# Optimization experiments

Measured on AMD Instinct MI355X. Metric: run time of the kernel, lower is better.

## Reference

```python
import jax, jax.numpy as jnp
import numpy as np

B, K, H, T, V = 32, 5, 512, 256, 5000
MAX_LEN = 64
SOS, EOS, PAD = 1, 2, 0
NEG = -1e9
ALPHA, MIN_LEN = 1.2, 5.0
SCALE = 1.0 / float(np.sqrt(H))


def setup_inputs() -> dict:
    key = jax.random.key(0)
    ks = jax.random.split(key, 5)
    s = 0.02
    return {
        "input_var": jnp.full((B, 1), SOS, dtype=jnp.int32),
        "encoder_outputs": jax.random.normal(ks[0], (B, T, H), dtype=jnp.float32),
        "emb_table": jax.random.normal(ks[1], (V, H), dtype=jnp.float32) * s,
        "w_ih": jax.random.normal(ks[2], (H, 3 * H), dtype=jnp.float32) * s,
        "w_hh": jax.random.normal(ks[3], (H, 3 * H), dtype=jnp.float32) * s,
        "w_out": jax.random.normal(ks[4], (2 * H, V), dtype=jnp.float32) * s,
        "k": K,
    }


def _gru_cell(x, h, w_ih, w_hh):
    iz, ir, inn = jnp.split(x @ w_ih, 3, axis=-1)
    hz, hr, hn = jnp.split(h @ w_hh, 3, axis=-1)
    z = jax.nn.sigmoid(iz + hz)
    r = jax.nn.sigmoid(ir + hr)
    n = jnp.tanh(inn + r * hn)
    return (1.0 - z) * n + z * h


def _forward_step(tok, h, enc, emb_table, w_ih, w_hh, w_out):
    # tok: [N] int, h: [N,H], enc: [N,T,H] -> (log-probs [N,V], new hidden [N,H])
    x = emb_table[tok]
    h = _gru_cell(x, h, w_ih, w_hh)
    att = jax.nn.softmax(jnp.einsum("nh,nth->nt", h, enc) * SCALE, axis=-1)
    ctx = jnp.einsum("nt,nth->nh", att, enc)
    logits = jnp.concatenate([h, ctx], axis=-1) @ w_out
    return jax.nn.log_softmax(logits, axis=-1), h


def reference(input_var, encoder_outputs, emb_table, w_ih, w_hh, w_out, k):
    bsz = encoder_outputs.shape[0]
    f32 = encoder_outputs.dtype

    # --- first step on un-inflated batch (hidden starts at zeros) ---
    h0 = jnp.zeros((bsz, H), dtype=f32)
    lp0, h1 = _forward_step(input_var[:, 0], h0, encoder_outputs,
                            emb_table, w_ih, w_hh, w_out)
    cum, beams = jax.lax.top_k(lp0, k)            # [B,k], [B,k]

    # inflate encoder states / hidden to beam-major layout [B*k, ...]
    enc_k = jnp.repeat(encoder_outputs, k, axis=0)   # [B*k,T,H]
    h = jnp.repeat(h1, k, axis=0)                    # [B*k,H]

    tokens = jnp.zeros((bsz, k, MAX_LEN), dtype=jnp.int32)
    tokens = tokens.at[:, :, 0].set(beams)
    finished = beams == EOS
    lengths = jnp.ones((bsz, k), dtype=jnp.int32)
    # finished beams may only extend with PAD at zero added log-prob
    pad_lp = jnp.where(jnp.arange(V) == PAD, 0.0, NEG).astype(f32)

    def body(carry, di):
        tokens, last, cum, h, finished, lengths = carry
        lp, h_new = _forward_step(last.reshape(-1), h, enc_k,
                                  emb_table, w_ih, w_hh, w_out)
        lp = lp.reshape(bsz, k, V)
        lp = jnp.where(finished[:, :, None], pad_lp[None, None, :], lp)
        # joint top-k over k*V candidates == per-beam topk(k) then topk over k^2
        cand = (cum[:, :, None] + lp).reshape(bsz, k * V)
        scores, idx = jax.lax.top_k(cand, k)      # [B,k]
        beam_ids = idx // V
        tok_ids = idx % V
        tokens = jnp.take_along_axis(tokens, beam_ids[:, :, None], axis=1)
        tokens = tokens.at[:, :, di].set(tok_ids)
        prev_fin = jnp.take_along_axis(finished, beam_ids, axis=1)
        lengths = jnp.take_along_axis(lengths, beam_ids, axis=1) + jnp.where(prev_fin, 0, 1)
        finished = prev_fin | (tok_ids == EOS)
        h = jnp.take_along_axis(h_new.reshape(bsz, k, H),
                                beam_ids[:, :, None], axis=1).reshape(bsz * k, H)
        return (tokens, tok_ids, scores, h, finished, lengths), None

    carry = (tokens, beams.astype(jnp.int32), cum, h, finished, lengths)
    (tokens, _, cum, _, finished, lengths), _ = jax.lax.scan(
        body, carry, jnp.arange(1, MAX_LEN))

    # length penalty on finished hypotheses, then pick best beam per batch
    penalty = ((MIN_LEN + lengths.astype(f32)) / (MIN_LEN + 1.0)) ** ALPHA
    sel = jnp.where(finished, cum / penalty, cum)
    best = jnp.argmax(sel, axis=1)
    hypothesis = jnp.take_along_axis(tokens, best[:, None, None], axis=1)[:, 0, :]
    return hypothesis, cum
```

## Files before the change

kernel.cpp:

```cpp
#include <hip/hip_runtime.h>
#include <math.h>

#define BB     32
#define KBM    5
#define NR     160
#define HD     512
#define TT     256
#define VV     5000
#define MAXLEN 64
#define EOSID  2
#define NEGV   (-1e9f)
#define NEGBIG (-3.0e38f)
#define SCALEF 0.04419417382415922f
#define NBLK   256
#define NTHR   512

typedef float v4f __attribute__((ext_vector_type(4)));

__device__ __forceinline__ float ld_sysf(const float* p) {
  return __hip_atomic_load(p, __ATOMIC_RELAXED, __HIP_MEMORY_SCOPE_SYSTEM);
}
__device__ __forceinline__ void st_sysf(float* p, float v) {
  __hip_atomic_store(p, v, __ATOMIC_RELAXED, __HIP_MEMORY_SCOPE_SYSTEM);
}
__device__ __forceinline__ int ld_sysi(const int* p) {
  return __hip_atomic_load(p, __ATOMIC_RELAXED, __HIP_MEMORY_SCOPE_SYSTEM);
}
__device__ __forceinline__ void st_sysi(int* p, int v) {
  __hip_atomic_store(p, v, __ATOMIC_RELAXED, __HIP_MEMORY_SCOPE_SYSTEM);
}
__device__ __forceinline__ v4f ld4_sys(const float* p) {
  v4f v;
  asm volatile("global_load_dwordx4 %0, %1, off sc0 sc1\n\ts_waitcnt vmcnt(0)"
               : "=v"(v) : "v"(p) : "memory");
  return v;
}
__device__ __forceinline__ void st4_sys(float* p, v4f v) {
  asm volatile("global_store_dwordx4 %0, %1, off sc0 sc1" :: "v"(p), "v"(v) : "memory");
}

__device__ __forceinline__ bool viBetter(float av, int ai, float bv, int bi) {
  return (av > bv) || (av == bv && ai < bi);
}

__device__ __forceinline__ void top5_insert(float tv[5], int ti[5], float x, int v) {
  if (!viBetter(x, v, tv[4], ti[4])) return;
  tv[4] = x; ti[4] = v;
#pragma unroll
  for (int q = 4; q > 0; q--) {
    if (viBetter(tv[q], ti[q], tv[q - 1], ti[q - 1])) {
      float tf = tv[q - 1]; int tx2 = ti[q - 1];
      tv[q - 1] = tv[q]; ti[q - 1] = ti[q];
      tv[q] = tf; ti[q] = tx2;
    } else break;
  }
}

template<int LEVELS>
__device__ __forceinline__ void bfly_argmax(float& v, int& i) {
#pragma unroll
  for (int d = 1; d < (1 << LEVELS); d <<= 1) {
    float ov = __shfl_xor(v, d);
    int oi = __shfl_xor(i, d);
    if (viBetter(ov, oi, v, i)) { v = ov; i = oi; }
  }
}

__global__ void k_zero(unsigned int* bar) {
  if (threadIdx.x < 320)
    __hip_atomic_store(&bar[threadIdx.x], 0u, __ATOMIC_RELAXED, __HIP_MEMORY_SCOPE_SYSTEM);
}

__launch_bounds__(NTHR, 1)
__global__ void k_persist(const int* __restrict__ input_var, const float* __restrict__ enc,
                          const float* __restrict__ emb, const float* __restrict__ w_ih,
                          const float* __restrict__ w_hh, const float* __restrict__ w_out,
                          float* __restrict__ out,
                          float* h, float* A_cat,
                          float* sumM, float* sumS, float* sumV, int* sumI,
                          int* last_tok, unsigned int* bar) {
  const int bid = blockIdx.x;
  const int tid = threadIdx.x;
  unsigned int ep = 0;

  __shared__ float sh_xs[32][40];
  __shared__ float sh_hs[32][40];
  __shared__ float sh_ws[6][32][32];
  __shared__ int   sh_toks[32];
  __shared__ float sh_h5[KBM][HD];
  __shared__ float sh_part[2][KBM][TT];
  __shared__ float sh_sc5[KBM][TT];
  __shared__ float sh_tmp5[KBM][TT];
  __shared__ float sh_as[32][72];
  __shared__ float sh_bs[64][136];
  __shared__ float sh_candV[KBM * KBM]; __shared__ int sh_candI[KBM * KBM];
  __shared__ int   sh_tokens[KBM][MAXLEN];
  __shared__ float sh_cum[KBM];
  __shared__ int   sh_fin[KBM]; __shared__ int sh_len[KBM];
  __shared__ float sh_oc[KBM];  __shared__ int sh_ofin[KBM]; __shared__ int sh_olen[KBM];
  __shared__ int   sh_ttmp[KBM * MAXLEN];
  __shared__ int   sh_selI[KBM]; __shared__ float sh_selV[KBM];

  auto gbar = [&]() {
    asm volatile("s_waitcnt vmcnt(0)" ::: "memory");
    __syncthreads();
    ep += 1;
    if (tid == 0) {
      __hip_atomic_fetch_add(&bar[(bid & 7) * 32], 1u, __ATOMIC_RELAXED,
                             __HIP_MEMORY_SCOPE_SYSTEM);
      if (bid == 0) {
        for (int c = 0; c < 8; c++) {
          while (__hip_atomic_load(&bar[c * 32], __ATOMIC_RELAXED,
                                   __HIP_MEMORY_SCOPE_SYSTEM) < ep * 32u) {
            __builtin_amdgcn_s_sleep(1);
          }
        }
        __hip_atomic_store(&bar[288], ep, __ATOMIC_RELAXED, __HIP_MEMORY_SCOPE_SYSTEM);
      } else {
        while (__hip_atomic_load(&bar[288], __ATOMIC_RELAXED,
                                 __HIP_MEMORY_SCOPE_SYSTEM) < ep) {
          __builtin_amdgcn_s_sleep(2);
        }
      }
    }
    __syncthreads();
  };

  if (bid < BB) {
    if (tid < KBM) { sh_cum[tid] = 0.f; sh_fin[tid] = 0; sh_len[tid] = 0; }
    for (int t = tid; t < KBM * MAXLEN; t += NTHR) sh_tokens[t >> 6][t & 63] = 0;
  }
  {
    int gidx = bid * NTHR + tid;
    v4f z4; z4[0] = z4[1] = z4[2] = z4[3] = 0.f;
    for (int i = gidx; i < NR * HD / 4; i += NBLK * NTHR) st4_sys(&h[i * 4], z4);
    for (int t = gidx; t < NR; t += NBLK * NTHR) st_sysi(&last_tok[t], input_var[t / KBM]);
  }
  gbar();

  for (int di = 0; di < MAXLEN; di++) {
    if (bid < 80) {
      const int bx = bid & 15, by = bid >> 4;
      const int i0 = bx * 32, n0 = by * 32;
      const int tx = tid & 31, ty = tid >> 5;
      if (tid < 32) sh_toks[tid] = ld_sysi(&last_tok[n0 + tid]);
      float acc[6][2];
#pragma unroll
      for (int g = 0; g < 6; g++) { acc[g][0] = 0.f; acc[g][1] = 0.f; }

      for (int k0 = 0; k0 < HD; k0 += 32) {
        __syncthreads();
#pragma unroll
        for (int p = 0; p < 4; p++) {
          int idx = tid + p * NTHR;
          if (idx < 256) {
            int r = idx >> 3, c4 = (idx & 7) * 4;
            *(v4f*)&sh_xs[r][c4] =
                *(const v4f*)&emb[(size_t)sh_toks[r] * HD + k0 + c4];
          } else if (idx < 512) {
            int r = (idx - 256) >> 3, c4 = ((idx - 256) & 7) * 4;
            *(v4f*)&sh_hs[r][c4] = ld4_sys(&h[(size_t)(n0 + r) * HD + k0 + c4]);
          } else {
            int widx = idx - 512;
            int g = widx >> 8, rem = widx & 255;
            int kk = rem >> 3, c4 = (rem & 7) * 4;
            const float* W = (g < 3) ? w_ih : w_hh;
            int gc = (g < 3) ? g : g - 3;
            *(v4f*)&sh_ws[g][kk][c4] =
                *(const v4f*)&W[(size_t)(k0 + kk) * 1536 + gc * HD + i0 + c4];
          }
        }
        __syncthreads();
#pragma unroll 8
        for (int k = 0; k < 32; k++) {
          float w0 = sh_ws[0][k][tx], w1 = sh_ws[1][k][tx], w2 = sh_ws[2][k][tx];
          float w3 = sh_ws[3][k][tx], w4 = sh_ws[4][k][tx], w5 = sh_ws[5][k][tx];
#pragma unroll
          for (int rr = 0; rr < 2; rr++) {
            float xv = sh_xs[ty * 2 + rr][k];
            float hv = sh_hs[ty * 2 + rr][k];
            acc[0][rr] += xv * w0; acc[1][rr] += xv * w1; acc[2][rr] += xv * w2;
            acc[3][rr] += hv * w3; acc[4][rr] += hv * w4; acc[5][rr] += hv * w5;
          }
        }
      }
#pragma unroll
      for (int rr = 0; rr < 2; rr++) {
        int n = n0 + ty * 2 + rr, i = i0 + tx;
        float hv = ld_sysf(&h[(size_t)n * HD + i]);
        float z = 1.f / (1.f + expf(-(acc[0][rr] + acc[3][rr])));
        float r = 1.f / (1.f + expf(-(acc[1][rr] + acc[4][rr])));
        float nn = tanhf(acc[2][rr] + r * acc[5][rr]);
        st_sysf(&A_cat[(size_t)n * 1024 + i], (1.f - z) * nn + z * hv);
      }
    }
    gbar();

    if (bid < BB) {
      const int b = bid;
      for (int idx = tid; idx < 640; idx += NTHR) {
        int j = idx >> 7, kc = (idx & 127) * 4;
        *(v4f*)&sh_h5[j][kc] = ld4_sys(&A_cat[(size_t)(b * KBM + j) * 1024 + kc]);
      }
      __syncthreads();
      {
        const int t = tid & 255, half = tid >> 8;
        const int kb = half * 256;
        float a[KBM];
#pragma unroll
        for (int j = 0; j < KBM; j++) a[j] = 0.f;
        const float* ep2 = enc + ((size_t)b * TT + t) * HD + kb;
#pragma unroll 4
        for (int k = 0; k < 256; k += 4) {
          v4f e = *(const v4f*)(ep2 + k);
#pragma unroll
          for (int j = 0; j < KBM; j++) {
            v4f hj = *(const v4f*)&sh_h5[j][kb + k];
            a[j] += hj[0] * e[0] + hj[1] * e[1] + hj[2] * e[2] + hj[3] * e[3];
          }
        }
#pragma unroll
        for (int j = 0; j < KBM; j++) sh_part[half][j][t] = a[j];
      }
      __syncthreads();
      if (tid < 256) {
#pragma unroll
        for (int j = 0; j < KBM; j++) {
          float sc = (sh_part[0][j][tid] + sh_part[1][j][tid]) * SCALEF;
          sh_sc5[j][tid] = sc;
          sh_tmp5[j][tid] = sc;
        }
      }
      __syncthreads();
      for (int off = 128; off > 0; off >>= 1) {
        if (tid < off) {
#pragma unroll
          for (int j = 0; j < KBM; j++)
            sh_tmp5[j][tid] = fmaxf(sh_tmp5[j][tid], sh_tmp5[j][tid + off]);
        }
        __syncthreads();
      }
      float mj[KBM];
#pragma unroll
      for (int j = 0; j < KBM; j++) mj[j] = sh_tmp5[j][0];
      __syncthreads();
      if (tid < 256) {
#pragma unroll
        for (int j = 0; j < KBM; j++) {
          float e = expf(sh_sc5[j][tid] - mj[j]);
          sh_sc5[j][tid] = e;
          sh_tmp5[j][tid] = e;
        }
      }
      __syncthreads();
      for (int off = 128; off > 0; off >>= 1) {
        if (tid < off) {
#pragma unroll
          for (int j = 0; j < KBM; j++) sh_tmp5[j][tid] += sh_tmp5[j][tid + off];
        }
        __syncthreads();
      }
      float Sj[KBM];
#pragma unroll
      for (int j = 0; j < KBM; j++) Sj[j] = sh_tmp5[j][0];
      __syncthreads();
      if (tid < 256) {
#pragma unroll
        for (int j = 0; j < KBM; j++) sh_sc5[j][tid] = sh_sc5[j][tid] / Sj[j];
      }
      __syncthreads();
      {
        float cx[KBM];
#pragma unroll
        for (int j = 0; j < KBM; j++) cx[j] = 0.f;
        const float* eb = enc + (size_t)b * TT * HD + tid;
#pragma unroll 4
        for (int t2 = 0; t2 < TT; t2++) {
          float e = eb[(size_t)t2 * HD];
#pragma unroll
          for (int j = 0; j < KBM; j++) cx[j] += sh_sc5[j][t2] * e;
        }
#pragma unroll
        for (int j = 0; j < KBM; j++)
          st_sysf(&A_cat[(size_t)(b * KBM + j) * 1024 + HD + tid], cx[j]);
      }
    }
    gbar();

    if (bid < 200) {
      const int bc = bid % 40, br = bid / 40;
      const int c0 = bc * 128, n0 = br * 32;
      const int tx = tid & 31, ty = tid >> 5;
      float acc[2][4];
#pragma unroll
      for (int rr = 0; rr < 2; rr++)
#pragma unroll
        for (int cc = 0; cc < 4; cc++) acc[rr][cc] = 0.f;

      for (int k0 = 0; k0 < 1024; k0 += 64) {
        __syncthreads();
#pragma unroll
        for (int p = 0; p < 4; p++) {
          int idx = tid + p * NTHR;
          int kk = idx >> 5, c4 = (idx & 31) * 4;
          int col = c0 + c4;
          v4f v;
          if (col + 3 < VV) v = *(const v4f*)&w_out[(size_t)(k0 + kk) * VV + col];
          else { v[0] = v[1] = v[2] = v[3] = 0.f; }
          *(v4f*)&sh_bs[kk][c4] = v;
        }
        {
          int r = tid >> 4, k4 = (tid & 15) * 4;
          *(v4f*)&sh_as[r][k4] = ld4_sys(&A_cat[(size_t)(n0 + r) * 1024 + k0 + k4]);
        }
        __syncthreads();
#pragma unroll 16
        for (int k = 0; k < 64; k++) {
          v4f bv = *(const v4f*)&sh_bs[k][tx * 4];
#pragma unroll
          for (int rr = 0; rr < 2; rr++) {
            float a = sh_as[ty * 2 + rr][k];
            acc[rr][0] += a * bv[0]; acc[rr][1] += a * bv[1];
            acc[rr][2] += a * bv[2]; acc[rr][3] += a * bv[3];
          }
        }
      }
#pragma unroll
      for (int rr = 0; rr < 2; rr++) {
        const int rowg = n0 + ty * 2 + rr;
        float vv[4]; int ci[4];
        float m = NEGBIG, s = 0.f;
#pragma unroll
        for (int cc = 0; cc < 4; cc++) {
          int c = c0 + tx * 4 + cc;
          ci[cc] = c;
          if (c < VV) {
            float x = acc[rr][cc];
            vv[cc] = x;
            float mn = fmaxf(m, x);
            s = s * expf(m - mn) + expf(x - mn);
            m = mn;
          } else {
            vv[cc] = NEGBIG;
          }
        }
#pragma unroll
        for (int d = 1; d < 32; d <<= 1) {
          float om = __shfl_xor(m, d), os = __shfl_xor(s, d);
          float mm = fmaxf(m, om);
          s = s * expf(m - mm) + os * expf(om - mm);
          m = mm;
        }
        float tv[5]; int ti[5];
#pragma unroll
        for (int q = 0; q < 5; q++) {
          float bvv = vv[0]; int bii = ci[0];
#pragma unroll
          for (int cc = 1; cc < 4; cc++)
            if (viBetter(vv[cc], ci[cc], bvv, bii)) { bvv = vv[cc]; bii = ci[cc]; }
          bfly_argmax<5>(bvv, bii);
          tv[q] = bvv; ti[q] = bii;
#pragma unroll
          for (int cc = 0; cc < 4; cc++)
            if (ci[cc] == bii) vv[cc] = -3.2e38f;
        }
        if ((tid & 31) == 0) {
          int base = rowg * 40 + bc;
          st_sysf(&sumM[base], m);
          st_sysf(&sumS[base], s);
#pragma unroll
          for (int q = 0; q < 5; q++) {
            st_sysf(&sumV[base * 5 + q], tv[q]);
            st_sysi(&sumI[base * 5 + q], ti[q]);
          }
        }
      }
    }
    gbar();

    if (bid < BB) {
      const int b = bid;
      if (tid < KBM) {
        sh_oc[tid] = sh_cum[tid]; sh_ofin[tid] = sh_fin[tid]; sh_olen[tid] = sh_len[tid];
      }
      for (int t = tid; t < KBM * MAXLEN; t += NTHR) sh_ttmp[t] = sh_tokens[t >> 6][t & 63];
      __syncthreads();

      const int w = tid >> 6, lane = tid & 63;
      const bool act = (di == 0) ? (w == 0) : (w < KBM);
      if (act) {
        const int j = (di == 0) ? 0 : w;
        if (di > 0 && sh_ofin[j]) {
          if (lane == 0) {
            float cj = sh_oc[j];
            sh_candV[j * KBM + 0] = cj;
            sh_candI[j * KBM + 0] = j * VV + 0;
#pragma unroll
            for (int q = 1; q < KBM; q++) {
              sh_candV[j * KBM + q] = cj + NEGV;
              sh_candI[j * KBM + q] = j * VV + q;
            }
          }
        } else {
          const int row = b * KBM + j;
          float m, s; float lv[5]; int li[5];
          if (lane < 40) {
            int base = row * 40 + lane;
            m = ld_sysf(&sumM[base]); s = ld_sysf(&sumS[base]);
#pragma unroll
            for (int q = 0; q < 5; q++) {
              lv[q] = ld_sysf(&sumV[base * 5 + q]);
              li[q] = ld_sysi(&sumI[base * 5 + q]);
            }
          } else {
            m = NEGBIG; s = 0.f;
#pragma unroll
            for (int q = 0; q < 5; q++) { lv[q] = NEGBIG; li[q] = 0x7fffffff; }
          }
#pragma unroll
          for (int d = 1; d < 64; d <<= 1) {
            float om = __shfl_xor(m, d), os = __shfl_xor(s, d);
            float mm = fmaxf(m, om);
            s = s * expf(m - mm) + os * expf(om - mm);
            m = mm;
          }
          float lse = m + logf(s);
          float cj = (di == 0) ? 0.f : sh_oc[j];
#pragma unroll
          for (int q = 0; q < 5; q++) {
            float bvv = lv[0]; int bii = li[0];
#pragma unroll
            for (int p = 1; p < 5; p++)
              if (viBetter(lv[p], li[p], bvv, bii)) { bvv = lv[p]; bii = li[p]; }
            bfly_argmax<6>(bvv, bii);
            if (lane == 0) {
              sh_candV[j * KBM + q] = cj + (bvv - lse);
              sh_candI[j * KBM + q] = j * VV + bii;
            }
#pragma unroll
            for (int p = 0; p < 5; p++)
              if (li[p] == bii) lv[p] = -3.2e38f;
          }
        }
      }
      __syncthreads();
      if (tid == 0) {
        if (di == 0) {
#pragma unroll
          for (int q = 0; q < KBM; q++) { sh_selV[q] = sh_candV[q]; sh_selI[q] = sh_candI[q]; }
        } else {
          float fv[5]; int fi[5];
#pragma unroll
          for (int q = 0; q < 5; q++) { fv[q] = -INFINITY; fi[q] = 0x7fffffff; }
          for (int t = 0; t < KBM * KBM; t++)
            top5_insert(fv, fi, sh_candV[t], sh_candI[t]);
#pragma unroll
          for (int q = 0; q < 5; q++) { sh_selV[q] = fv[q]; sh_selI[q] = fi[q]; }
        }
      }
      __syncthreads();
      if (tid < KBM) {
        int p = tid, idx = sh_selI[p];
        int bm = idx / VV, tk = idx - bm * VV;
        int pf = sh_ofin[bm];
        sh_cum[p] = sh_selV[p];
        sh_len[p] = sh_olen[bm] + (pf ? 0 : 1);
        sh_fin[p] = (pf || tk == EOSID) ? 1 : 0;
        st_sysi(&last_tok[b * KBM + p], tk);
      }
      for (int t = tid; t < KBM * MAXLEN; t += NTHR) {
        int p = t >> 6, pos = t & 63;
        int idx = sh_selI[p]; int bm = idx / VV; int tk = idx - bm * VV;
        sh_tokens[p][pos] = (pos == di) ? tk : sh_ttmp[bm * MAXLEN + pos];
      }
      for (int idx = tid; idx < 640; idx += NTHR) {
        int p = idx >> 7, e4 = (idx & 127) * 4;
        int bm = sh_selI[p] / VV;
        v4f v = ld4_sys(&A_cat[(size_t)(b * KBM + bm) * 1024 + e4]);
        st4_sys(&h[(size_t)(b * KBM + p) * HD + e4], v);
      }
    }
    gbar();
  }

  if (bid < BB) {
    const int b = bid;
    if (tid == 0) {
      int best = 0; float bv = -INFINITY;
#pragma unroll
      for (int jj = 0; jj < KBM; jj++) {
        float c = sh_cum[jj];
        float pen = powf((5.0f + (float)sh_len[jj]) / 6.0f, 1.2f);
        float sel = sh_fin[jj] ? (c / pen) : c;
        if (sel > bv) { bv = sel; best = jj; }
      }
      sh_selI[0] = best;
    }
    __syncthreads();
    if (tid < MAXLEN) out[b * MAXLEN + tid] = (float)sh_tokens[sh_selI[0]][tid];
    if (tid < KBM) out[BB * MAXLEN + b * KBM + tid] = sh_cum[tid];
  }
}

extern "C" void kernel_launch(void* const* d_in, const int* in_sizes, int n_in,
                              void* d_out, int out_size, void* d_ws, size_t ws_size,
                              hipStream_t stream) {
  (void)in_sizes; (void)n_in; (void)out_size; (void)ws_size;
  const int*   input_var = (const int*)d_in[0];
  const float* enc       = (const float*)d_in[1];
  const float* emb       = (const float*)d_in[2];
  const float* w_ih      = (const float*)d_in[3];
  const float* w_hh      = (const float*)d_in[4];
  const float* w_out     = (const float*)d_in[5];
  float* out = (float*)d_out;

  float* h       = (float*)d_ws;
  float* A_cat   = h + (size_t)NR * HD;
  float* sumM    = A_cat + (size_t)NR * 1024;
  float* sumS    = sumM + NR * 40;
  float* sumV    = sumS + NR * 40;
  int*   sumI    = (int*)(sumV + NR * 40 * 5);
  int*   last_tok = sumI + NR * 40 * 5;
  unsigned int* bar = (unsigned int*)(last_tok + NR);

  k_zero<<<1, 512, 0, stream>>>(bar);
  k_persist<<<NBLK, NTHR, 0, stream>>>(input_var, enc, emb, w_ih, w_hh, w_out, out,
                                       h, A_cat, sumM, sumS, sumV, sumI,
                                       last_tok, bar);
}
```

Before: 9.874 ms.

## Batch system-scope loads before one waitcnt and pack beam summaries into vectors

Previously each system-coherent 16-byte load waited for its own completion. Now all loads for a tile stage are issued first, then a single s_waitcnt binds them, so memory latency overlaps across loads in the GRU, attention and output-projection tiles. The per-column softmax/top-5 summaries move from four scalar arrays into one 12-float record written and read with three vector accesses. The GRU's previous-hidden value is taken from the shared tile instead of a separate global load, and the context loop unroll goes from 4 to 8. The inline-asm binding depends on the compiler keeping the register constraints correct, and one extra __syncthreads is added before the hidden-state copy.

```diff
diff --git a/kernel.cpp b/kernel.cpp
--- a/kernel.cpp
+++ b/kernel.cpp
@@ -29,11 +29,29 @@
 __device__ __forceinline__ void st_sysi(int* p, int v) {
   __hip_atomic_store(p, v, __ATOMIC_RELAXED, __HIP_MEMORY_SCOPE_SYSTEM);
 }
-__device__ __forceinline__ v4f ld4_sys(const float* p) {
+
+__device__ __forceinline__ v4f ld4_issue_sys(const float* p) {
   v4f v;
-  asm volatile("global_load_dwordx4 %0, %1, off sc0 sc1\n\ts_waitcnt vmcnt(0)"
-               : "=v"(v) : "v"(p) : "memory");
+  asm volatile("global_load_dwordx4 %0, %1, off sc0 sc1" : "=v"(v) : "v"(p));
   return v;
+}
+__device__ __forceinline__ v4f ld4_issue(const float* p) {
+  v4f v;
+  asm volatile("global_load_dwordx4 %0, %1, off" : "=v"(v) : "v"(p));
+  return v;
+}
+__device__ __forceinline__ void vm_bind2(v4f& a, v4f& b) {
+  asm volatile("s_waitcnt vmcnt(0)" : "+v"(a), "+v"(b) :: "memory");
+}
+__device__ __forceinline__ void vm_bind3(v4f& a, v4f& b, v4f& c) {
+  asm volatile("s_waitcnt vmcnt(0)" : "+v"(a), "+v"(b), "+v"(c) :: "memory");
+}
+__device__ __forceinline__ void vm_bind4(v4f& a, v4f& b, v4f& c, v4f& d) {
+  asm volatile("s_waitcnt vmcnt(0)" : "+v"(a), "+v"(b), "+v"(c), "+v"(d) :: "memory");
+}
+__device__ __forceinline__ void vm_bind5(v4f& a, v4f& b, v4f& c, v4f& d, v4f& e) {
+  asm volatile("s_waitcnt vmcnt(0)"
+               : "+v"(a), "+v"(b), "+v"(c), "+v"(d), "+v"(e) :: "memory");
 }
 __device__ __forceinline__ void st4_sys(float* p, v4f v) {
   asm volatile("global_store_dwordx4 %0, %1, off sc0 sc1" :: "v"(p), "v"(v) : "memory");
@@ -76,8 +94,7 @@
                           const float* __restrict__ emb, const float* __restrict__ w_ih,
                           const float* __restrict__ w_hh, const float* __restrict__ w_out,
                           float* __restrict__ out,
-                          float* h, float* A_cat,
-                          float* sumM, float* sumS, float* sumV, int* sumI,
+                          float* h, float* A_cat, float* summ,
                           int* last_tok, unsigned int* bar) {
   const int bid = blockIdx.x;
   const int tid = threadIdx.x;
@@ -147,30 +164,46 @@
       float acc[6][2];
 #pragma unroll
       for (int g = 0; g < 6; g++) { acc[g][0] = 0.f; acc[g][1] = 0.f; }
+      float hcap0 = 0.f, hcap1 = 0.f;
 
       for (int k0 = 0; k0 < HD; k0 += 32) {
         __syncthreads();
-#pragma unroll
-        for (int p = 0; p < 4; p++) {
-          int idx = tid + p * NTHR;
-          if (idx < 256) {
-            int r = idx >> 3, c4 = (idx & 7) * 4;
-            *(v4f*)&sh_xs[r][c4] =
-                *(const v4f*)&emb[(size_t)sh_toks[r] * HD + k0 + c4];
-          } else if (idx < 512) {
-            int r = (idx - 256) >> 3, c4 = ((idx - 256) & 7) * 4;
-            *(v4f*)&sh_hs[r][c4] = ld4_sys(&h[(size_t)(n0 + r) * HD + k0 + c4]);
-          } else {
-            int widx = idx - 512;
-            int g = widx >> 8, rem = widx & 255;
-            int kk = rem >> 3, c4 = (rem & 7) * 4;
-            const float* W = (g < 3) ? w_ih : w_hh;
-            int gc = (g < 3) ? g : g - 3;
-            *(v4f*)&sh_ws[g][kk][c4] =
-                *(const v4f*)&W[(size_t)(k0 + kk) * 1536 + gc * HD + i0 + c4];
-          }
-        }
+        v4f v0, v1, v2, v3;
+        if (tid < 256) {
+          int r = tid >> 3, c4 = (tid & 7) * 4;
+          v0 = ld4_issue(&emb[(size_t)sh_toks[r] * HD + k0 + c4]);
+        } else {
+          int r = (tid - 256) >> 3, c4 = ((tid - 256) & 7) * 4;
+          v0 = ld4_issue_sys(&h[(size_t)(n0 + r) * HD + k0 + c4]);
+        }
+        int gW[3], kW[3], cW[3];
+#pragma unroll
+        for (int p = 0; p < 3; p++) {
+          int widx = tid + p * 512;
+          int g = widx >> 8, rem = widx & 255;
+          int kk = rem >> 3, c4 = (rem & 7) * 4;
+          const float* W = (g < 3) ? w_ih : w_hh;
+          int gc = (g < 3) ? g : g - 3;
+          v4f t = ld4_issue(&W[(size_t)(k0 + kk) * 1536 + gc * HD + i0 + c4]);
+          if (p == 0) v1 = t; else if (p == 1) v2 = t; else v3 = t;
+          gW[p] = g; kW[p] = kk; cW[p] = c4;
+        }
+        vm_bind4(v0, v1, v2, v3);
+        if (tid < 256) {
+          int r = tid >> 3, c4 = (tid & 7) * 4;
+          *(v4f*)&sh_xs[r][c4] = v0;
+        } else {
+          int r = (tid - 256) >> 3, c4 = ((tid - 256) & 7) * 4;
+          *(v4f*)&sh_hs[r][c4] = v0;
+        }
+        *(v4f*)&sh_ws[gW[0]][kW[0]][cW[0]] = v1;
+        *(v4f*)&sh_ws[gW[1]][kW[1]][cW[1]] = v2;
+        *(v4f*)&sh_ws[gW[2]][kW[2]][cW[2]] = v3;
         __syncthreads();
+        if (k0 == i0) {
+          hcap0 = sh_hs[ty * 2 + 0][tx];
+          hcap1 = sh_hs[ty * 2 + 1][tx];
+        }
 #pragma unroll 8
         for (int k = 0; k < 32; k++) {
           float w0 = sh_ws[0][k][tx], w1 = sh_ws[1][k][tx], w2 = sh_ws[2][k][tx];
@@ -187,7 +220,7 @@
 #pragma unroll
       for (int rr = 0; rr < 2; rr++) {
         int n = n0 + ty * 2 + rr, i = i0 + tx;
-        float hv = ld_sysf(&h[(size_t)n * HD + i]);
+        float hv = rr ? hcap1 : hcap0;
         float z = 1.f / (1.f + expf(-(acc[0][rr] + acc[3][rr])));
         float r = 1.f / (1.f + expf(-(acc[1][rr] + acc[4][rr])));
         float nn = tanhf(acc[2][rr] + r * acc[5][rr]);
@@ -198,9 +231,20 @@
 
     if (bid < BB) {
       const int b = bid;
-      for (int idx = tid; idx < 640; idx += NTHR) {
-        int j = idx >> 7, kc = (idx & 127) * 4;
-        *(v4f*)&sh_h5[j][kc] = ld4_sys(&A_cat[(size_t)(b * KBM + j) * 1024 + kc]);
+      {
+        v4f x0, x1 = {};
+        int j0 = tid >> 7, kc0 = (tid & 127) * 4;
+        x0 = ld4_issue_sys(&A_cat[(size_t)(b * KBM + j0) * 1024 + kc0]);
+        if (tid < 128) {
+          int idx = tid + 512;
+          x1 = ld4_issue_sys(&A_cat[(size_t)(b * KBM + (idx >> 7)) * 1024 + (idx & 127) * 4]);
+        }
+        vm_bind2(x0, x1);
+        *(v4f*)&sh_h5[j0][kc0] = x0;
+        if (tid < 128) {
+          int idx = tid + 512;
+          *(v4f*)&sh_h5[idx >> 7][(idx & 127) * 4] = x1;
+        }
       }
       __syncthreads();
       {
@@ -274,7 +318,7 @@
 #pragma unroll
         for (int j = 0; j < KBM; j++) cx[j] = 0.f;
         const float* eb = enc + (size_t)b * TT * HD + tid;
-#pragma unroll 4
+#pragma unroll 8
         for (int t2 = 0; t2 < TT; t2++) {
           float e = eb[(size_t)t2 * HD];
 #pragma unroll
@@ -299,20 +343,26 @@
 
       for (int k0 = 0; k0 < 1024; k0 += 64) {
         __syncthreads();
+        v4f a0, b0, b1, b2, b3;
+        const int ar = tid >> 4, ak4 = (tid & 15) * 4;
+        a0 = ld4_issue_sys(&A_cat[(size_t)(n0 + ar) * 1024 + k0 + ak4]);
+        int kkB[4], cB[4];
 #pragma unroll
         for (int p = 0; p < 4; p++) {
-          int idx = tid + p * NTHR;
+          int idx = tid + p * 512;
           int kk = idx >> 5, c4 = (idx & 31) * 4;
           int col = c0 + c4;
-          v4f v;
-          if (col + 3 < VV) v = *(const v4f*)&w_out[(size_t)(k0 + kk) * VV + col];
-          else { v[0] = v[1] = v[2] = v[3] = 0.f; }
-          *(v4f*)&sh_bs[kk][c4] = v;
-        }
-        {
-          int r = tid >> 4, k4 = (tid & 15) * 4;
-          *(v4f*)&sh_as[r][k4] = ld4_sys(&A_cat[(size_t)(n0 + r) * 1024 + k0 + k4]);
-        }
+          v4f t; t[0] = t[1] = t[2] = t[3] = 0.f;
+          if (col + 3 < VV) t = ld4_issue(&w_out[(size_t)(k0 + kk) * VV + col]);
+          if (p == 0) b0 = t; else if (p == 1) b1 = t; else if (p == 2) b2 = t; else b3 = t;
+          kkB[p] = kk; cB[p] = c4;
+        }
+        vm_bind5(a0, b0, b1, b2, b3);
+        *(v4f*)&sh_as[ar][ak4] = a0;
+        *(v4f*)&sh_bs[kkB[0]][cB[0]] = b0;
+        *(v4f*)&sh_bs[kkB[1]][cB[1]] = b1;
+        *(v4f*)&sh_bs[kkB[2]][cB[2]] = b2;
+        *(v4f*)&sh_bs[kkB[3]][cB[3]] = b3;
         __syncthreads();
 #pragma unroll 16
         for (int k = 0; k < 64; k++) {
@@ -365,14 +415,14 @@
             if (ci[cc] == bii) vv[cc] = -3.2e38f;
         }
         if ((tid & 31) == 0) {
-          int base = rowg * 40 + bc;
-          st_sysf(&sumM[base], m);
-          st_sysf(&sumS[base], s);
-#pragma unroll
-          for (int q = 0; q < 5; q++) {
-            st_sysf(&sumV[base * 5 + q], tv[q]);
-            st_sysi(&sumI[base * 5 + q], ti[q]);
-          }
+          float* base = &summ[((size_t)rowg * 40 + bc) * 12];
+          v4f p0v, p1v, p2v;
+          p0v[0] = m; p0v[1] = s; p0v[2] = tv[0]; p0v[3] = tv[1];
+          p1v[0] = tv[2]; p1v[1] = tv[3]; p1v[2] = tv[4];
+          p1v[3] = __int_as_float(ti[0]);
+          p2v[0] = __int_as_float(ti[1]); p2v[1] = __int_as_float(ti[2]);
+          p2v[2] = __int_as_float(ti[3]); p2v[3] = __int_as_float(ti[4]);
+          st4_sys(base, p0v); st4_sys(base + 4, p1v); st4_sys(base + 8, p2v);
         }
       }
     }
@@ -405,13 +455,16 @@
           const int row = b * KBM + j;
           float m, s; float lv[5]; int li[5];
           if (lane < 40) {
-            int base = row * 40 + lane;
-            m = ld_sysf(&sumM[base]); s = ld_sysf(&sumS[base]);
-#pragma unroll
-            for (int q = 0; q < 5; q++) {
-              lv[q] = ld_sysf(&sumV[base * 5 + q]);
-              li[q] = ld_sysi(&sumI[base * 5 + q]);
-            }
+            const float* base = &summ[((size_t)row * 40 + lane) * 12];
+            v4f s0 = ld4_issue_sys(base);
+            v4f s1 = ld4_issue_sys(base + 4);
+            v4f s2 = ld4_issue_sys(base + 8);
+            vm_bind3(s0, s1, s2);
+            m = s0[0]; s = s0[1];
+            lv[0] = s0[2]; lv[1] = s0[3]; lv[2] = s1[0]; lv[3] = s1[1]; lv[4] = s1[2];
+            li[0] = __float_as_int(s1[3]);
+            li[1] = __float_as_int(s2[0]); li[2] = __float_as_int(s2[1]);
+            li[3] = __float_as_int(s2[2]); li[4] = __float_as_int(s2[3]);
           } else {
             m = NEGBIG; s = 0.f;
 #pragma unroll
@@ -473,11 +526,19 @@
         int idx = sh_selI[p]; int bm = idx / VV; int tk = idx - bm * VV;
         sh_tokens[p][pos] = (pos == di) ? tk : sh_ttmp[bm * MAXLEN + pos];
       }
-      for (int idx = tid; idx < 640; idx += NTHR) {
-        int p = idx >> 7, e4 = (idx & 127) * 4;
-        int bm = sh_selI[p] / VV;
-        v4f v = ld4_sys(&A_cat[(size_t)(b * KBM + bm) * 1024 + e4]);
-        st4_sys(&h[(size_t)(b * KBM + p) * HD + e4], v);
+      __syncthreads();
+      {
+        int p0 = tid >> 7, e40 = (tid & 127) * 4;
+        int bm0 = sh_selI[p0] / VV;
+        v4f y0 = ld4_issue_sys(&A_cat[(size_t)(b * KBM + bm0) * 1024 + e40]);
+        v4f y1 = {};
+        if (tid < 128) {
+          int bm1 = sh_selI[4] / VV;
+          y1 = ld4_issue_sys(&A_cat[(size_t)(b * KBM + bm1) * 1024 + tid * 4]);
+        }
+        vm_bind2(y0, y1);
+        st4_sys(&h[(size_t)(b * KBM + p0) * HD + e40], y0);
+        if (tid < 128) st4_sys(&h[(size_t)(b * KBM + 4) * HD + tid * 4], y1);
       }
     }
     gbar();
@@ -516,15 +577,11 @@
 
   float* h       = (float*)d_ws;
   float* A_cat   = h + (size_t)NR * HD;
-  float* sumM    = A_cat + (size_t)NR * 1024;
-  float* sumS    = sumM + NR * 40;
-  float* sumV    = sumS + NR * 40;
-  int*   sumI    = (int*)(sumV + NR * 40 * 5);
-  int*   last_tok = sumI + NR * 40 * 5;
+  float* summ    = A_cat + (size_t)NR * 1024;
+  int*   last_tok = (int*)(summ + (size_t)NR * 40 * 12);
   unsigned int* bar = (unsigned int*)(last_tok + NR);
 
   k_zero<<<1, 512, 0, stream>>>(bar);
   k_persist<<<NBLK, NTHR, 0, stream>>>(input_var, enc, emb, w_ih, w_hh, w_out, out,
-                                       h, A_cat, sumM, sumS, sumV, sumI,
-                                       last_tok, bar);
-}
+                                       h, A_cat, summ, last_tok, bar);
+}
```

Result: faster. 9.458 ms (-4.2%).
